# Performance work log

Measured on AMD Instinct MI355X. Metric: run time of the kernel, lower is better.

The kernel has to match this reference:

```python
import jax, jax.numpy as jnp
import numpy as np

B = 4096
N0 = 784          # MNIST input
L0 = 263          # fc0: Gather chain 784 -> 256 (ELU after each)
L2 = 121          # fc2: Gather chain 256 -> 12 (ELU after each); final Gather 12 -> 10 has no ELU


def _win3(x):
    # x: (B, N) -> (B, N-2, 3) sliding windows of width 3
    return jnp.stack([x[:, :-2], x[:, 1:-1], x[:, 2:]], axis=-1)


def setup_inputs() -> dict:
    key = jax.random.key(0)
    kx, k0, k1, k2, k3, k4 = jax.random.split(key, 6)
    s = 0.75  # keeps activation variance roughly stable through ~380 ELU glia layers
    x = jax.random.normal(kx, (B, N0), jnp.float32)
    W0 = jax.random.normal(k0, (L0, 782, 3), jnp.float32) * s
    m0 = np.arange(782)[None, :] < (780 - 2 * np.arange(L0))[:, None]
    W0 = W0 * jnp.asarray(m0[..., None], jnp.float32)  # zero out rows past each layer's out size
    Ws = jax.random.normal(k1, (256, 3), jnp.float32) * s
    bs = jax.random.normal(k2, (256,), jnp.float32) * 0.1
    W2 = jax.random.normal(k3, (L2, 254, 3), jnp.float32) * s
    m2 = np.arange(254)[None, :] < (252 - 2 * np.arange(L2))[:, None]
    W2 = W2 * jnp.asarray(m2[..., None], jnp.float32)
    Wlast = jax.random.normal(k4, (10, 3), jnp.float32) * s
    return {"x": x, "W0": W0, "Ws": Ws, "bs": bs, "W2": W2, "Wlast": Wlast}


def reference(x, W0, Ws, bs, W2, Wlast):
    def gather_step(h, W):
        # locally-connected width-3 Gather (out = in - 2, bias=False) + ELU.
        # Invalid tail rows of W are zero, so padded positions stay exactly 0
        # (ELU(0)=0) and never contaminate valid windows.
        y = jax.nn.elu(jnp.einsum('bjk,jk->bj', _win3(h), W))
        return jnp.pad(y, ((0, 0), (0, 2))), None

    # fc0: 263 Gather+ELU layers, 784 -> 256 (valid prefix of fixed-width state)
    h, _ = jax.lax.scan(gather_step, x, W0)
    h = h[:, :256]
    # fc1: Slide(256) + ELU -- same-size width-3 locally connected layer, zero-padded window, bias
    hp = jnp.pad(h, ((0, 0), (1, 1)))
    h = jax.nn.elu(jnp.einsum('bjk,jk->bj', _win3(hp), Ws) + bs)
    # fc2: 121 Gather+ELU layers, 256 -> 12
    h, _ = jax.lax.scan(gather_step, h, W2)
    # final Gather(12): 12 -> 10, no ELU
    logits = jnp.einsum('bjk,jk->bj', _win3(h[:, :12]), Wlast)
    return jax.nn.log_softmax(logits, axis=1)
```

## Files before the change

kernel.cpp:

```cpp
#include <hip/hip_runtime.h>
#include <math.h>


#define G 2

template<int HI>
__device__ __forceinline__ float2 pk_mul_b(float2 a, float2 w) {
    float2 d;
    if constexpr (HI)
        asm("v_pk_mul_f32 %0, %1, %2 op_sel:[0,1] op_sel_hi:[1,1]"
            : "=v"(d) : "v"(a), "v"(w));
    else
        asm("v_pk_mul_f32 %0, %1, %2 op_sel_hi:[1,0]"
            : "=v"(d) : "v"(a), "v"(w));
    return d;
}
template<int HI>
__device__ __forceinline__ float2 pk_fma_b(float2 a, float2 w, float2 c) {
    float2 d;
    if constexpr (HI)
        asm("v_pk_fma_f32 %0, %1, %2, %3 op_sel:[0,1,0] op_sel_hi:[1,1,1]"
            : "=v"(d) : "v"(a), "v"(w), "v"(c));
    else
        asm("v_pk_fma_f32 %0, %1, %2, %3 op_sel_hi:[1,0,1]"
            : "=v"(d) : "v"(a), "v"(w), "v"(c));
    return d;
}
__device__ __forceinline__ float2 pk_mul2(float2 a, float2 b) {
    float2 d;
    asm("v_pk_mul_f32 %0, %1, %2" : "=v"(d) : "v"(a), "v"(b));
    return d;
}
__device__ __forceinline__ float vexp2(float x) {
    float d;
    asm("v_exp_f32 %0, %1" : "=v"(d) : "v"(x));
    return d;
}

__device__ __forceinline__ float elu_f(float a) {
    return a > 0.0f ? a : (__expf(a) - 1.0f);
}

template<int K, int I, int NW>
__device__ __forceinline__ void slot_run(float2 (&h)[K], const float2 (&w)[NW],
                                         float2 e0, float2 e1, float2 l2e) {
    if constexpr (I < K) {
        float2 x1, x2;
        if constexpr (I + 1 < K) x1 = h[I + 1]; else x1 = e0;
        if constexpr (I + 2 < K) x2 = h[I + 2];
        else if constexpr (I + 2 == K) x2 = e0;
        else x2 = e1;
        float2 acc = pk_mul_b<(3 * I + 2) & 1>(x2, w[(3 * I + 2) >> 1]);
        acc = pk_fma_b<(3 * I + 1) & 1>(x1, w[(3 * I + 1) >> 1], acc);
        acc = pk_fma_b<(3 * I) & 1>(h[I], w[(3 * I) >> 1], acc);
        float2 t = pk_mul2(acc, l2e);
        float ex = vexp2(t.x) - 1.0f;
        float ey = vexp2(t.y) - 1.0f;
        h[I].x = acc.x > 0.0f ? acc.x : ex;
        h[I].y = acc.y > 0.0f ? acc.y : ey;
        slot_run<K, I + 1, NW>(h, w, e0, e1, l2e);
    }
}

template<int K, int NW>
__device__ __forceinline__ void scan_layer_pk(float2 (&h)[K], const float2 (&w)[NW],
                                              float2 l2e) {
    float2 e0, e1;
    e0.x = __shfl_down(h[0].x, 1); e0.y = __shfl_down(h[0].y, 1);
    if constexpr (K >= 2) { e1.x = __shfl_down(h[1].x, 1); e1.y = __shfl_down(h[1].y, 1); }
    else                  { e1.x = __shfl_down(h[0].x, 2); e1.y = __shfl_down(h[0].y, 2); }
    slot_run<K, 0, NW>(h, w, e0, e1, l2e);
}

template<int NC>
__device__ __forceinline__ void load_wt2(float2 (&w)[2 * NC], const float4* __restrict__ Tp,
                                         int lr) {
#pragma unroll
    for (int c = 0; c < NC; ++c) {
        float4 v = Tp[(size_t)lr * (NC * 64) + c * 64];
        w[2 * c]     = make_float2(v.x, v.y);
        w[2 * c + 1] = make_float2(v.z, v.w);
    }
}

template<int K, int NC>
__device__ __forceinline__ void scan_phase_pk(const float* __restrict__ Tphase, int nl,
                                              int lane, float2 (&h)[K], float2 l2e) {
    const float4* __restrict__ Tp = reinterpret_cast<const float4*>(Tphase) + lane;
    float2 wa[2 * NC], wb[2 * NC];
    load_wt2<NC>(wa, Tp, 0);
    int l = 0;
    for (; l + 2 <= nl; l += 2) {
        load_wt2<NC>(wb, Tp, l + 1);
        scan_layer_pk<K>(h, wa, l2e);
        if (l + 3 <= nl) load_wt2<NC>(wa, Tp, l + 2);
        scan_layer_pk<K>(h, wb, l2e);
    }
    if (l < nl) scan_layer_pk<K>(h, wa, l2e);
}

template<int KA, int KB>
__device__ __forceinline__ void repack_pk(float2 (&a)[KA], float2 (&n)[KB],
                                          float2* lds, int lane) {
    __syncthreads();
#pragma unroll
    for (int i = 0; i < KA; ++i) lds[KA * lane + i] = a[i];
    __syncthreads();
#pragma unroll
    for (int i = 0; i < KB; ++i) n[i] = lds[KB * lane + i];
    __syncthreads();
}

__device__ __forceinline__ void stage2_pk(float2 (&h)[5], const float* __restrict__ Ws,
                                          const float* __restrict__ bs, int lane) {
#pragma unroll
    for (int i = 0; i < 5; ++i)
        if (5 * lane + i > 255) h[i] = make_float2(0.f, 0.f);
    float w0[5], w1[5], w2[5], bb[5];
#pragma unroll
    for (int i = 0; i < 5; ++i) {
        int j = 5 * lane + i;
        bool v = j < 256;
        w0[i] = v ? Ws[3 * j + 0] : 0.f;
        w1[i] = v ? Ws[3 * j + 1] : 0.f;
        w2[i] = v ? Ws[3 * j + 2] : 0.f;
        bb[i] = v ? bs[j] : 0.f;
    }
    float2 p, q;
    p.x = __shfl_up(h[4].x, 1); p.y = __shfl_up(h[4].y, 1);
    if (lane == 0) p = make_float2(0.f, 0.f);
    q.x = __shfl_down(h[0].x, 1); q.y = __shfl_down(h[0].y, 1);
    float2 y[5];
#pragma unroll
    for (int i = 0; i < 5; ++i) {
        float2 xm = (i == 0) ? p : h[i - 1];
        float2 xp = (i == 4) ? q : h[i + 1];
        float ax = fmaf(xm.x, w0[i], fmaf(h[i].x, w1[i], fmaf(xp.x, w2[i], bb[i])));
        float ay = fmaf(xm.y, w0[i], fmaf(h[i].y, w1[i], fmaf(xp.y, w2[i], bb[i])));
        y[i].x = elu_f(ax);
        y[i].y = elu_f(ay);
    }
#pragma unroll
    for (int i = 0; i < 5; ++i) h[i] = y[i];
}

__device__ __forceinline__ void emit_row(float v, const float* __restrict__ Wl,
                                         float* __restrict__ out, int row, int lane) {
    float n1 = __shfl_down(v, 1);
    float n2 = __shfl_down(v, 2);
    float lg = 0.0f;
    if (lane < 10)
        lg = fmaf(v, Wl[3 * lane], fmaf(n1, Wl[3 * lane + 1], n2 * Wl[3 * lane + 2]));
    float t = (lane < 10) ? lg : -1e30f;
#pragma unroll
    for (int d = 1; d < 16; d <<= 1) t = fmaxf(t, __shfl_xor(t, d));
    float e = (lane < 10) ? __expf(lg - t) : 0.0f;
    float s = e;
#pragma unroll
    for (int d = 1; d < 16; d <<= 1) s += __shfl_xor(s, d);
    float lse = t + __logf(s);
    if (lane < 10) out[(size_t)row * 10 + lane] = lg - lse;
}

#define T_TOTAL 531712

__global__ __launch_bounds__(256)
void reorder_w(const float* __restrict__ W0, const float* __restrict__ W2,
               float* __restrict__ T) {
    int idx = blockIdx.x * 256 + threadIdx.x;
    if (idx >= T_TOTAL) return;
    int base, l0, K, NC, s1;
    if      (idx < 17920)  { base = 0;      l0 = 0;   K = 13; NC = 10; s1 = 1; }
    else if (idx < 91648)  { base = 17920;  l0 = 7;   K = 12; NC = 9;  s1 = 1; }
    else if (idx < 165376) { base = 91648;  l0 = 39;  K = 11; NC = 9;  s1 = 1; }
    else if (idx < 230912) { base = 165376; l0 = 71;  K = 10; NC = 8;  s1 = 1; }
    else if (idx < 288256) { base = 230912; l0 = 103; K = 9;  NC = 7;  s1 = 1; }
    else if (idx < 337408) { base = 288256; l0 = 135; K = 8;  NC = 6;  s1 = 1; }
    else if (idx < 386560) { base = 337408; l0 = 167; K = 7;  NC = 6;  s1 = 1; }
    else if (idx < 427520) { base = 386560; l0 = 199; K = 6;  NC = 5;  s1 = 1; }
    else if (idx < 460288) { base = 427520; l0 = 231; K = 5;  NC = 4;  s1 = 1; }
    else if (idx < 484096) { base = 460288; l0 = 0;   K = 4;  NC = 3;  s1 = 0; }
    else if (idx < 508672) { base = 484096; l0 = 31;  K = 3;  NC = 3;  s1 = 0; }
    else if (idx < 525056) { base = 508672; l0 = 63;  K = 2;  NC = 2;  s1 = 0; }
    else                   { base = 525056; l0 = 95;  K = 1;  NC = 1;  s1 = 0; }
    const float* Wsrc = s1 ? W0 : W2;
    int lstride = s1 ? 2346 : 762;
    int rel  = idx - base;
    int perL = NC * 256;
    int lr   = rel / perL;
    int r2   = rel - lr * perL;
    int c    = r2 >> 8;
    int ln   = (r2 >> 2) & 63;
    int f    = r2 & 3;
    int elem = 4 * c + f;
    float v = 0.0f;
    if (elem < 3 * K) {
        int b = 3 * K * ln;
        if (b + 3 * K > lstride) b = lstride - 3 * K;
        v = Wsrc[(size_t)(l0 + lr) * lstride + b + elem];
    }
    T[idx] = v;
}

__global__ __launch_bounds__(64)
void pg_kernel_pk(const float* __restrict__ x,  const float* __restrict__ Ws,
                  const float* __restrict__ bs, const float* __restrict__ Wlast,
                  const float* __restrict__ T,  float* __restrict__ out)
{
    __shared__ float2 lds2[13 * 64];
    const int lane = threadIdx.x;
    const int rowA = blockIdx.x * G;
    const int rowB = rowA + 1;
    const float2 l2e = make_float2(1.44269504088896340736f, 1.44269504088896340736f);

    float2 h13[13];
#pragma unroll
    for (int i = 0; i < 13; ++i) {
        int p = 13 * lane + i;
        h13[i].x = (p < 784) ? x[(size_t)rowA * 784 + p] : 0.0f;
        h13[i].y = (p < 784) ? x[(size_t)rowB * 784 + p] : 0.0f;
    }

    scan_phase_pk<13, 10>(T + 0,      7,  lane, h13, l2e);
    float2 h12[12]; repack_pk<13, 12>(h13, h12, lds2, lane);
    scan_phase_pk<12, 9>(T + 17920,   32, lane, h12, l2e);
    float2 h11[11]; repack_pk<12, 11>(h12, h11, lds2, lane);
    scan_phase_pk<11, 9>(T + 91648,   32, lane, h11, l2e);
    float2 h10[10]; repack_pk<11, 10>(h11, h10, lds2, lane);
    scan_phase_pk<10, 8>(T + 165376,  32, lane, h10, l2e);
    float2 h9[9];   repack_pk<10, 9>(h10, h9, lds2, lane);
    scan_phase_pk<9, 7>(T + 230912,   32, lane, h9, l2e);
    float2 h8[8];   repack_pk<9, 8>(h9, h8, lds2, lane);
    scan_phase_pk<8, 6>(T + 288256,   32, lane, h8, l2e);
    float2 h7[7];   repack_pk<8, 7>(h8, h7, lds2, lane);
    scan_phase_pk<7, 6>(T + 337408,   32, lane, h7, l2e);
    float2 h6[6];   repack_pk<7, 6>(h7, h6, lds2, lane);
    scan_phase_pk<6, 5>(T + 386560,   32, lane, h6, l2e);
    float2 h5[5];   repack_pk<6, 5>(h6, h5, lds2, lane);
    scan_phase_pk<5, 4>(T + 427520,   32, lane, h5, l2e);

    stage2_pk(h5, Ws, bs, lane);

    float2 h4[4];   repack_pk<5, 4>(h5, h4, lds2, lane);
    scan_phase_pk<4, 3>(T + 460288,   31, lane, h4, l2e);
    float2 h3[3];   repack_pk<4, 3>(h4, h3, lds2, lane);
    scan_phase_pk<3, 3>(T + 484096,   32, lane, h3, l2e);
    float2 h2[2];   repack_pk<3, 2>(h3, h2, lds2, lane);
    scan_phase_pk<2, 2>(T + 508672,   32, lane, h2, l2e);
    float2 h1[1];   repack_pk<2, 1>(h2, h1, lds2, lane);
    scan_phase_pk<1, 1>(T + 525056,   26, lane, h1, l2e);

    emit_row(h1[0].x, Wlast, out, rowA, lane);
    emit_row(h1[0].y, Wlast, out, rowB, lane);
}

template<int K>
__device__ __forceinline__ void scan_layer_s(float (&h)[K], const float (&w)[3 * K]) {
    float e0 = __shfl_down(h[0], 1);
    float e1;
    if constexpr (K >= 2) e1 = __shfl_down(h[1], 1);
    else                  e1 = __shfl_down(h[0], 2);
#pragma unroll
    for (int i = 0; i < K; ++i) {
        float x1 = (i + 1 < K) ? h[i + 1] : e0;
        float x2 = (i + 2 < K) ? h[i + 2] : ((i + 2 == K) ? e0 : e1);
        float a = fmaf(h[i], w[3 * i], fmaf(x1, w[3 * i + 1], x2 * w[3 * i + 2]));
        h[i] = elu_f(a);
    }
}
template<int K>
__device__ __forceinline__ void scan_phase_s(const float* __restrict__ W, int lstride,
                                             int l0, int l1, int lane,
                                             float (&hA)[K], float (&hB)[K]) {
    int base = 3 * K * lane;
    if (base + 3 * K > lstride) base = lstride - 3 * K;
    const float* __restrict__ Wp = W + (size_t)l0 * lstride + base;
    float wa[3 * K];
    for (int l = l0; l < l1; ++l) {
#pragma unroll
        for (int j = 0; j < 3 * K; ++j) wa[j] = Wp[j];
        scan_layer_s<K>(hA, wa);
        scan_layer_s<K>(hB, wa);
        Wp += lstride;
    }
}
template<int KA, int KB>
__device__ __forceinline__ void repack_s(float (&aA)[KA], float (&aB)[KA],
                                         float (&nA)[KB], float (&nB)[KB],
                                         float* lds, int lane) {
    __syncthreads();
#pragma unroll
    for (int i = 0; i < KA; ++i) lds[KA * lane + i] = aA[i];
    __syncthreads();
#pragma unroll
    for (int i = 0; i < KB; ++i) nA[i] = lds[KB * lane + i];
    __syncthreads();
#pragma unroll
    for (int i = 0; i < KA; ++i) lds[KA * lane + i] = aB[i];
    __syncthreads();
#pragma unroll
    for (int i = 0; i < KB; ++i) nB[i] = lds[KB * lane + i];
    __syncthreads();
}
__global__ __launch_bounds__(64)
void pg_kernel_d(const float* __restrict__ x,  const float* __restrict__ W0,
                 const float* __restrict__ Ws, const float* __restrict__ bs,
                 const float* __restrict__ W2, const float* __restrict__ Wlast,
                 float* __restrict__ out)
{
    __shared__ float lds[13 * 64];
    const int lane = threadIdx.x;
    const int rowA = blockIdx.x * G;
    const int rowB = rowA + 1;
    float a13[13], b13[13];
#pragma unroll
    for (int i = 0; i < 13; ++i) {
        int p = 13 * lane + i;
        a13[i] = (p < 784) ? x[(size_t)rowA * 784 + p] : 0.0f;
        b13[i] = (p < 784) ? x[(size_t)rowB * 784 + p] : 0.0f;
    }
    scan_phase_s<13>(W0, 2346, 0, 71, lane, a13, b13);
    float a10[10], b10[10]; repack_s<13, 10>(a13, b13, a10, b10, lds, lane);
    scan_phase_s<10>(W0, 2346, 71, 167, lane, a10, b10);
    float a7[7], b7[7];     repack_s<10, 7>(a10, b10, a7, b7, lds, lane);
    scan_phase_s<7>(W0, 2346, 167, 231, lane, a7, b7);
    float a5[5], b5[5];     repack_s<7, 5>(a7, b7, a5, b5, lds, lane);
    scan_phase_s<5>(W0, 2346, 231, 263, lane, a5, b5);
    {
        float2 hp[5];
#pragma unroll
        for (int i = 0; i < 5; ++i) hp[i] = make_float2(a5[i], b5[i]);
        stage2_pk(hp, Ws, bs, lane);
#pragma unroll
        for (int i = 0; i < 5; ++i) { a5[i] = hp[i].x; b5[i] = hp[i].y; }
    }
    float a4[4], b4[4];     repack_s<5, 4>(a5, b5, a4, b4, lds, lane);
    scan_phase_s<4>(W2, 762, 0, 31, lane, a4, b4);
    float a3[3], b3[3];     repack_s<4, 3>(a4, b4, a3, b3, lds, lane);
    scan_phase_s<3>(W2, 762, 31, 63, lane, a3, b3);
    float a2_[2], b2_[2];   repack_s<3, 2>(a3, b3, a2_, b2_, lds, lane);
    scan_phase_s<2>(W2, 762, 63, 95, lane, a2_, b2_);
    float a1[1], b1[1];     repack_s<2, 1>(a2_, b2_, a1, b1, lds, lane);
    scan_phase_s<1>(W2, 762, 95, 121, lane, a1, b1);
    emit_row(a1[0], Wlast, out, rowA, lane);
    emit_row(b1[0], Wlast, out, rowB, lane);
}

extern "C" void kernel_launch(void* const* d_in, const int* in_sizes, int n_in,
                              void* d_out, int out_size, void* d_ws, size_t ws_size,
                              hipStream_t stream) {
    const float* x     = (const float*)d_in[0];
    const float* W0    = (const float*)d_in[1];
    const float* Ws    = (const float*)d_in[2];
    const float* bs    = (const float*)d_in[3];
    const float* W2    = (const float*)d_in[4];
    const float* Wlast = (const float*)d_in[5];
    float* out = (float*)d_out;

    if (ws_size >= (size_t)T_TOTAL * sizeof(float)) {
        float* T = (float*)d_ws;
        reorder_w<<<(T_TOTAL + 255) / 256, 256, 0, stream>>>(W0, W2, T);
        pg_kernel_pk<<<4096 / G, 64, 0, stream>>>(x, Ws, bs, Wlast, T, out);
    } else {
        pg_kernel_d<<<4096 / G, 64, 0, stream>>>(x, W0, Ws, bs, W2, Wlast, out);
    }
}
```

Measured before the change: 245.6 us.

## Process one batch row per wavefront with scalar FMAs instead of packed pairs

The main kernel now gives each 64-lane block a single batch row instead of two, and drops the inline-asm packed v_pk_fma/v_pk_mul path in favour of plain scalar fmaf and __expf for ELU. The grid doubles to 4096 blocks, which gives the scheduler more independent waves to hide the serial layer-to-layer latency. In exchange, every weight load and shuffle is now shared by only one row instead of two, so weight traffic and shuffle count per row double and the packed-math throughput is lost.

```diff
diff --git a/kernel.cpp b/kernel.cpp
--- a/kernel.cpp
+++ b/kernel.cpp
@@ -2,106 +2,55 @@
 #include <math.h>
 
 
-#define G 2
-
-template<int HI>
-__device__ __forceinline__ float2 pk_mul_b(float2 a, float2 w) {
-    float2 d;
-    if constexpr (HI)
-        asm("v_pk_mul_f32 %0, %1, %2 op_sel:[0,1] op_sel_hi:[1,1]"
-            : "=v"(d) : "v"(a), "v"(w));
-    else
-        asm("v_pk_mul_f32 %0, %1, %2 op_sel_hi:[1,0]"
-            : "=v"(d) : "v"(a), "v"(w));
-    return d;
-}
-template<int HI>
-__device__ __forceinline__ float2 pk_fma_b(float2 a, float2 w, float2 c) {
-    float2 d;
-    if constexpr (HI)
-        asm("v_pk_fma_f32 %0, %1, %2, %3 op_sel:[0,1,0] op_sel_hi:[1,1,1]"
-            : "=v"(d) : "v"(a), "v"(w), "v"(c));
-    else
-        asm("v_pk_fma_f32 %0, %1, %2, %3 op_sel_hi:[1,0,1]"
-            : "=v"(d) : "v"(a), "v"(w), "v"(c));
-    return d;
-}
-__device__ __forceinline__ float2 pk_mul2(float2 a, float2 b) {
-    float2 d;
-    asm("v_pk_mul_f32 %0, %1, %2" : "=v"(d) : "v"(a), "v"(b));
-    return d;
-}
-__device__ __forceinline__ float vexp2(float x) {
-    float d;
-    asm("v_exp_f32 %0, %1" : "=v"(d) : "v"(x));
-    return d;
-}
-
 __device__ __forceinline__ float elu_f(float a) {
     return a > 0.0f ? a : (__expf(a) - 1.0f);
 }
 
-template<int K, int I, int NW>
-__device__ __forceinline__ void slot_run(float2 (&h)[K], const float2 (&w)[NW],
-                                         float2 e0, float2 e1, float2 l2e) {
-    if constexpr (I < K) {
-        float2 x1, x2;
-        if constexpr (I + 1 < K) x1 = h[I + 1]; else x1 = e0;
-        if constexpr (I + 2 < K) x2 = h[I + 2];
-        else if constexpr (I + 2 == K) x2 = e0;
-        else x2 = e1;
-        float2 acc = pk_mul_b<(3 * I + 2) & 1>(x2, w[(3 * I + 2) >> 1]);
-        acc = pk_fma_b<(3 * I + 1) & 1>(x1, w[(3 * I + 1) >> 1], acc);
-        acc = pk_fma_b<(3 * I) & 1>(h[I], w[(3 * I) >> 1], acc);
-        float2 t = pk_mul2(acc, l2e);
-        float ex = vexp2(t.x) - 1.0f;
-        float ey = vexp2(t.y) - 1.0f;
-        h[I].x = acc.x > 0.0f ? acc.x : ex;
-        h[I].y = acc.y > 0.0f ? acc.y : ey;
-        slot_run<K, I + 1, NW>(h, w, e0, e1, l2e);
-    }
-}
-
 template<int K, int NW>
-__device__ __forceinline__ void scan_layer_pk(float2 (&h)[K], const float2 (&w)[NW],
-                                              float2 l2e) {
-    float2 e0, e1;
-    e0.x = __shfl_down(h[0].x, 1); e0.y = __shfl_down(h[0].y, 1);
-    if constexpr (K >= 2) { e1.x = __shfl_down(h[1].x, 1); e1.y = __shfl_down(h[1].y, 1); }
-    else                  { e1.x = __shfl_down(h[0].x, 2); e1.y = __shfl_down(h[0].y, 2); }
-    slot_run<K, 0, NW>(h, w, e0, e1, l2e);
-}
-
-template<int NC>
-__device__ __forceinline__ void load_wt2(float2 (&w)[2 * NC], const float4* __restrict__ Tp,
-                                         int lr) {
+__device__ __forceinline__ void scan_layer_1(float (&h)[K], const float (&w)[NW]) {
+    static_assert(NW >= 3 * K, "weight array too small");
+    float e0 = __shfl_down(h[0], 1);
+    float e1;
+    if constexpr (K >= 2) e1 = __shfl_down(h[1], 1);
+    else                  e1 = __shfl_down(h[0], 2);
+#pragma unroll
+    for (int i = 0; i < K; ++i) {
+        float x1 = (i + 1 < K) ? h[i + 1] : e0;
+        float x2 = (i + 2 < K) ? h[i + 2] : ((i + 2 == K) ? e0 : e1);
+        float a = fmaf(h[i], w[3 * i], fmaf(x1, w[3 * i + 1], x2 * w[3 * i + 2]));
+        h[i] = elu_f(a);
+    }
+}
+
+template<int NC, int NW>
+__device__ __forceinline__ void load_wt(float (&w)[NW], const float4* __restrict__ Tp,
+                                        int lr) {
 #pragma unroll
     for (int c = 0; c < NC; ++c) {
         float4 v = Tp[(size_t)lr * (NC * 64) + c * 64];
-        w[2 * c]     = make_float2(v.x, v.y);
-        w[2 * c + 1] = make_float2(v.z, v.w);
+        w[4 * c + 0] = v.x; w[4 * c + 1] = v.y; w[4 * c + 2] = v.z; w[4 * c + 3] = v.w;
     }
 }
 
 template<int K, int NC>
-__device__ __forceinline__ void scan_phase_pk(const float* __restrict__ Tphase, int nl,
-                                              int lane, float2 (&h)[K], float2 l2e) {
+__device__ __forceinline__ void scan_phase_1(const float* __restrict__ Tphase, int nl,
+                                             int lane, float (&h)[K]) {
     const float4* __restrict__ Tp = reinterpret_cast<const float4*>(Tphase) + lane;
-    float2 wa[2 * NC], wb[2 * NC];
-    load_wt2<NC>(wa, Tp, 0);
+    float wa[4 * NC], wb[4 * NC];
+    load_wt<NC>(wa, Tp, 0);
     int l = 0;
     for (; l + 2 <= nl; l += 2) {
-        load_wt2<NC>(wb, Tp, l + 1);
-        scan_layer_pk<K>(h, wa, l2e);
-        if (l + 3 <= nl) load_wt2<NC>(wa, Tp, l + 2);
-        scan_layer_pk<K>(h, wb, l2e);
-    }
-    if (l < nl) scan_layer_pk<K>(h, wa, l2e);
+        load_wt<NC>(wb, Tp, l + 1);
+        scan_layer_1<K>(h, wa);
+        if (l + 3 <= nl) load_wt<NC>(wa, Tp, l + 2);
+        scan_layer_1<K>(h, wb);
+    }
+    if (l < nl) scan_layer_1<K>(h, wa);
 }
 
 template<int KA, int KB>
-__device__ __forceinline__ void repack_pk(float2 (&a)[KA], float2 (&n)[KB],
-                                          float2* lds, int lane) {
+__device__ __forceinline__ void repack1(float (&a)[KA], float (&n)[KB],
+                                        float* lds, int lane) {
     __syncthreads();
 #pragma unroll
     for (int i = 0; i < KA; ++i) lds[KA * lane + i] = a[i];
@@ -111,11 +60,11 @@
     __syncthreads();
 }
 
-__device__ __forceinline__ void stage2_pk(float2 (&h)[5], const float* __restrict__ Ws,
-                                          const float* __restrict__ bs, int lane) {
+__device__ __forceinline__ void stage2_1(float (&h)[5], const float* __restrict__ Ws,
+                                         const float* __restrict__ bs, int lane) {
 #pragma unroll
     for (int i = 0; i < 5; ++i)
-        if (5 * lane + i > 255) h[i] = make_float2(0.f, 0.f);
+        if (5 * lane + i > 255) h[i] = 0.0f;
     float w0[5], w1[5], w2[5], bb[5];
 #pragma unroll
     for (int i = 0; i < 5; ++i) {
@@ -126,19 +75,14 @@
         w2[i] = v ? Ws[3 * j + 2] : 0.f;
         bb[i] = v ? bs[j] : 0.f;
     }
-    float2 p, q;
-    p.x = __shfl_up(h[4].x, 1); p.y = __shfl_up(h[4].y, 1);
-    if (lane == 0) p = make_float2(0.f, 0.f);
-    q.x = __shfl_down(h[0].x, 1); q.y = __shfl_down(h[0].y, 1);
-    float2 y[5];
+    float p = __shfl_up(h[4], 1); if (lane == 0) p = 0.0f;
+    float q = __shfl_down(h[0], 1);
+    float y[5];
 #pragma unroll
     for (int i = 0; i < 5; ++i) {
-        float2 xm = (i == 0) ? p : h[i - 1];
-        float2 xp = (i == 4) ? q : h[i + 1];
-        float ax = fmaf(xm.x, w0[i], fmaf(h[i].x, w1[i], fmaf(xp.x, w2[i], bb[i])));
-        float ay = fmaf(xm.y, w0[i], fmaf(h[i].y, w1[i], fmaf(xp.y, w2[i], bb[i])));
-        y[i].x = elu_f(ax);
-        y[i].y = elu_f(ay);
+        float xm = (i == 0) ? p : h[i - 1];
+        float xp = (i == 4) ? q : h[i + 1];
+        y[i] = elu_f(fmaf(xm, w0[i], fmaf(h[i], w1[i], fmaf(xp, w2[i], bb[i]))));
     }
 #pragma unroll
     for (int i = 0; i < 5; ++i) h[i] = y[i];
@@ -203,71 +147,54 @@
 }
 
 __global__ __launch_bounds__(64)
-void pg_kernel_pk(const float* __restrict__ x,  const float* __restrict__ Ws,
-                  const float* __restrict__ bs, const float* __restrict__ Wlast,
-                  const float* __restrict__ T,  float* __restrict__ out)
+void pg_kernel_1(const float* __restrict__ x,  const float* __restrict__ Ws,
+                 const float* __restrict__ bs, const float* __restrict__ Wlast,
+                 const float* __restrict__ T,  float* __restrict__ out)
 {
-    __shared__ float2 lds2[13 * 64];
+    __shared__ float lds[13 * 64];
     const int lane = threadIdx.x;
-    const int rowA = blockIdx.x * G;
-    const int rowB = rowA + 1;
-    const float2 l2e = make_float2(1.44269504088896340736f, 1.44269504088896340736f);
-
-    float2 h13[13];
+    const int row  = blockIdx.x;
+    const float* __restrict__ xr = x + (size_t)row * 784;
+
+    float h13[13];
 #pragma unroll
     for (int i = 0; i < 13; ++i) {
         int p = 13 * lane + i;
-        h13[i].x = (p < 784) ? x[(size_t)rowA * 784 + p] : 0.0f;
-        h13[i].y = (p < 784) ? x[(size_t)rowB * 784 + p] : 0.0f;
-    }
-
-    scan_phase_pk<13, 10>(T + 0,      7,  lane, h13, l2e);
-    float2 h12[12]; repack_pk<13, 12>(h13, h12, lds2, lane);
-    scan_phase_pk<12, 9>(T + 17920,   32, lane, h12, l2e);
-    float2 h11[11]; repack_pk<12, 11>(h12, h11, lds2, lane);
-    scan_phase_pk<11, 9>(T + 91648,   32, lane, h11, l2e);
-    float2 h10[10]; repack_pk<11, 10>(h11, h10, lds2, lane);
-    scan_phase_pk<10, 8>(T + 165376,  32, lane, h10, l2e);
-    float2 h9[9];   repack_pk<10, 9>(h10, h9, lds2, lane);
-    scan_phase_pk<9, 7>(T + 230912,   32, lane, h9, l2e);
-    float2 h8[8];   repack_pk<9, 8>(h9, h8, lds2, lane);
-    scan_phase_pk<8, 6>(T + 288256,   32, lane, h8, l2e);
-    float2 h7[7];   repack_pk<8, 7>(h8, h7, lds2, lane);
-    scan_phase_pk<7, 6>(T + 337408,   32, lane, h7, l2e);
-    float2 h6[6];   repack_pk<7, 6>(h7, h6, lds2, lane);
-    scan_phase_pk<6, 5>(T + 386560,   32, lane, h6, l2e);
-    float2 h5[5];   repack_pk<6, 5>(h6, h5, lds2, lane);
-    scan_phase_pk<5, 4>(T + 427520,   32, lane, h5, l2e);
-
-    stage2_pk(h5, Ws, bs, lane);
-
-    float2 h4[4];   repack_pk<5, 4>(h5, h4, lds2, lane);
-    scan_phase_pk<4, 3>(T + 460288,   31, lane, h4, l2e);
-    float2 h3[3];   repack_pk<4, 3>(h4, h3, lds2, lane);
-    scan_phase_pk<3, 3>(T + 484096,   32, lane, h3, l2e);
-    float2 h2[2];   repack_pk<3, 2>(h3, h2, lds2, lane);
-    scan_phase_pk<2, 2>(T + 508672,   32, lane, h2, l2e);
-    float2 h1[1];   repack_pk<2, 1>(h2, h1, lds2, lane);
-    scan_phase_pk<1, 1>(T + 525056,   26, lane, h1, l2e);
-
-    emit_row(h1[0].x, Wlast, out, rowA, lane);
-    emit_row(h1[0].y, Wlast, out, rowB, lane);
-}
-
-template<int K>
-__device__ __forceinline__ void scan_layer_s(float (&h)[K], const float (&w)[3 * K]) {
-    float e0 = __shfl_down(h[0], 1);
-    float e1;
-    if constexpr (K >= 2) e1 = __shfl_down(h[1], 1);
-    else                  e1 = __shfl_down(h[0], 2);
-#pragma unroll
-    for (int i = 0; i < K; ++i) {
-        float x1 = (i + 1 < K) ? h[i + 1] : e0;
-        float x2 = (i + 2 < K) ? h[i + 2] : ((i + 2 == K) ? e0 : e1);
-        float a = fmaf(h[i], w[3 * i], fmaf(x1, w[3 * i + 1], x2 * w[3 * i + 2]));
-        h[i] = elu_f(a);
-    }
-}
+        h13[i] = (p < 784) ? xr[p] : 0.0f;
+    }
+
+    scan_phase_1<13, 10>(T + 0,      7,  lane, h13);
+    float h12[12]; repack1<13, 12>(h13, h12, lds, lane);
+    scan_phase_1<12, 9>(T + 17920,   32, lane, h12);
+    float h11[11]; repack1<12, 11>(h12, h11, lds, lane);
+    scan_phase_1<11, 9>(T + 91648,   32, lane, h11);
+    float h10[10]; repack1<11, 10>(h11, h10, lds, lane);
+    scan_phase_1<10, 8>(T + 165376,  32, lane, h10);
+    float h9[9];   repack1<10, 9>(h10, h9, lds, lane);
+    scan_phase_1<9, 7>(T + 230912,   32, lane, h9);
+    float h8[8];   repack1<9, 8>(h9, h8, lds, lane);
+    scan_phase_1<8, 6>(T + 288256,   32, lane, h8);
+    float h7[7];   repack1<8, 7>(h8, h7, lds, lane);
+    scan_phase_1<7, 6>(T + 337408,   32, lane, h7);
+    float h6[6];   repack1<7, 6>(h7, h6, lds, lane);
+    scan_phase_1<6, 5>(T + 386560,   32, lane, h6);
+    float h5[5];   repack1<6, 5>(h6, h5, lds, lane);
+    scan_phase_1<5, 4>(T + 427520,   32, lane, h5);
+
+    stage2_1(h5, Ws, bs, lane);
+
+    float h4[4];   repack1<5, 4>(h5, h4, lds, lane);
+    scan_phase_1<4, 3>(T + 460288,   31, lane, h4);
+    float h3[3];   repack1<4, 3>(h4, h3, lds, lane);
+    scan_phase_1<3, 3>(T + 484096,   32, lane, h3);
+    float h2[2];   repack1<3, 2>(h3, h2, lds, lane);
+    scan_phase_1<2, 2>(T + 508672,   32, lane, h2);
+    float h1[1];   repack1<2, 1>(h2, h1, lds, lane);
+    scan_phase_1<1, 1>(T + 525056,   26, lane, h1);
+
+    emit_row(h1[0], Wlast, out, row, lane);
+}
+
 template<int K>
 __device__ __forceinline__ void scan_phase_s(const float* __restrict__ W, int lstride,
                                              int l0, int l1, int lane,
@@ -279,8 +206,8 @@
     for (int l = l0; l < l1; ++l) {
 #pragma unroll
         for (int j = 0; j < 3 * K; ++j) wa[j] = Wp[j];
-        scan_layer_s<K>(hA, wa);
-        scan_layer_s<K>(hB, wa);
+        scan_layer_1<K>(hA, wa);
+        scan_layer_1<K>(hB, wa);
         Wp += lstride;
     }
 }
@@ -310,7 +237,7 @@
 {
     __shared__ float lds[13 * 64];
     const int lane = threadIdx.x;
-    const int rowA = blockIdx.x * G;
+    const int rowA = blockIdx.x * 2;
     const int rowB = rowA + 1;
     float a13[13], b13[13];
 #pragma unroll
@@ -326,14 +253,8 @@
     scan_phase_s<7>(W0, 2346, 167, 231, lane, a7, b7);
     float a5[5], b5[5];     repack_s<7, 5>(a7, b7, a5, b5, lds, lane);
     scan_phase_s<5>(W0, 2346, 231, 263, lane, a5, b5);
-    {
-        float2 hp[5];
-#pragma unroll
-        for (int i = 0; i < 5; ++i) hp[i] = make_float2(a5[i], b5[i]);
-        stage2_pk(hp, Ws, bs, lane);
-#pragma unroll
-        for (int i = 0; i < 5; ++i) { a5[i] = hp[i].x; b5[i] = hp[i].y; }
-    }
+    stage2_1(a5, Ws, bs, lane);
+    stage2_1(b5, Ws, bs, lane);
     float a4[4], b4[4];     repack_s<5, 4>(a5, b5, a4, b4, lds, lane);
     scan_phase_s<4>(W2, 762, 0, 31, lane, a4, b4);
     float a3[3], b3[3];     repack_s<4, 3>(a4, b4, a3, b3, lds, lane);
@@ -360,8 +281,8 @@
     if (ws_size >= (size_t)T_TOTAL * sizeof(float)) {
         float* T = (float*)d_ws;
         reorder_w<<<(T_TOTAL + 255) / 256, 256, 0, stream>>>(W0, W2, T);
-        pg_kernel_pk<<<4096 / G, 64, 0, stream>>>(x, Ws, bs, Wlast, T, out);
+        pg_kernel_1<<<4096, 64, 0, stream>>>(x, Ws, bs, Wlast, T, out);
     } else {
-        pg_kernel_d<<<4096 / G, 64, 0, stream>>>(x, W0, Ws, bs, W2, Wlast, out);
-    }
-}
+        pg_kernel_d<<<2048, 64, 0, stream>>>(x, W0, Ws, bs, W2, Wlast, out);
+    }
+}
```

New measurement: 305.2 us. 24.3% more time.
